# Performance work log

Hardware: AMD Instinct MI355X
Metric: run time of the kernel (lower is better)

The kernel has to match this reference:

```python
import jax, jax.numpy as jnp
import numpy as np

N = 100_000      # nodes
E = 1_250_000    # edges (avg degree ~12.5)
D_IN, D_H, D_OUT = 64, 64, 64


def setup_inputs() -> dict:
    key = jax.random.key(0)
    ks = jax.random.split(key, 7)
    x = jax.random.normal(ks[0], (N, D_IN), dtype=jnp.float32)
    edge_index = jax.random.randint(ks[1], (2, E), 0, N, dtype=jnp.int32)
    edge_weight = jax.random.uniform(ks[2], (E,), dtype=jnp.float32)
    # GCNConv linear weights: PyG lin stores [out, in], applied as x @ W.T; bias added after aggregation.
    W1 = jax.random.normal(ks[3], (D_H, D_IN), dtype=jnp.float32) * (1.0 / np.sqrt(D_IN))
    b1 = jax.random.normal(ks[4], (D_H,), dtype=jnp.float32) * 0.01
    W2 = jax.random.normal(ks[5], (D_OUT, D_H), dtype=jnp.float32) * (1.0 / np.sqrt(D_H))
    b2 = jax.random.normal(ks[6], (D_OUT,), dtype=jnp.float32) * 0.01
    return {"x": x, "edge_index": edge_index, "edge_weight": edge_weight,
            "W1": W1, "b1": b1, "W2": W2, "b2": b2}


def _gcn_conv(x, src, dst, w, W, b, n_nodes):
    # PyG GCNConv: add self-loops (weight 1), symmetric normalization, linear, scatter-add, +bias.
    deg = jax.ops.segment_sum(w, dst, num_segments=n_nodes) + 1.0  # +1 from self-loop
    dis = jnp.where(deg > 0, jax.lax.rsqrt(deg), 0.0)              # deg^{-1/2}
    coef = dis[src] * w * dis[dst]                                 # per-edge norm, [E]
    h = x @ W.T                                                    # [N, out]
    agg = jax.ops.segment_sum(h[src] * coef[:, None], dst, num_segments=n_nodes)
    agg = agg + h * (dis * dis)[:, None]                           # self-loop: dis_i * 1 * dis_i
    return agg + b


def reference(x, edge_index, edge_weight, W1, b1, W2, b2):
    n = x.shape[0]
    src, dst = edge_index[0], edge_index[1]
    h = _gcn_conv(x, src, dst, edge_weight, W1, b1, n)
    h = jax.nn.relu(h)
    # dropout p=0.0 -> identity
    return _gcn_conv(h, src, dst, edge_weight, W2, b2, n)
```

## Files before the change

### kernel.cpp

```cpp
#include <hip/hip_runtime.h>


typedef unsigned int u32;
typedef unsigned short u16;

#define NBKT 256
#define LSH 9
#define BNODES 512
#define SRCBITS 17
#define SRCMASK ((1u << SRCBITS) - 1u)

__device__ inline u16 f2bf(float f) {
  u32 u = __float_as_uint(f);
  u32 r = u + 0x7FFFu + ((u >> 16) & 1u);
  return (u16)(r >> 16);
}
__device__ inline float bf_lo(u32 p) { return __uint_as_float(p << 16); }
__device__ inline float bf_hi(u32 p) { return __uint_as_float(p & 0xFFFF0000u); }

__device__ inline u32 blockscan256_excl(u32 val, u32* wsum) {
  int lane = threadIdx.x & 63, wv = threadIdx.x >> 6;
  u32 inc = val;
  #pragma unroll
  for (int d = 1; d < 64; d <<= 1) {
    u32 t = __shfl_up(inc, d);
    if (lane >= d) inc += t;
  }
  if (lane == 63) wsum[wv] = inc;
  __syncthreads();
  u32 off = 0;
  #pragma unroll
  for (int i = 0; i < 4; ++i) if (i < wv) off += wsum[i];
  return off + inc - val;
}

__global__ void k_bin(const int* __restrict__ ei, u32* __restrict__ blockcnt,
                      int E, int chunk) {
  __shared__ u32 hist[NBKT];
  if (threadIdx.x < NBKT) hist[threadIdx.x] = 0u;
  __syncthreads();
  int e0 = blockIdx.x * chunk;
  int e1 = min(E, e0 + chunk);
  for (int e = e0 + (threadIdx.x << 1); e < e1; e += 512) {
    if (e + 1 < e1) {
      int2 dd = *(const int2*)(ei + E + e);
      atomicAdd(&hist[dd.x >> LSH], 1u);
      atomicAdd(&hist[dd.y >> LSH], 1u);
    } else {
      atomicAdd(&hist[ei[E + e] >> LSH], 1u);
    }
  }
  __syncthreads();
  if (threadIdx.x < NBKT)
    blockcnt[threadIdx.x * 256 + blockIdx.x] = hist[threadIdx.x];
}

__global__ void k_scan_rows(u32* __restrict__ blockcnt, u32* __restrict__ bucket_total) {
  int wid = blockIdx.x * 4 + (threadIdx.x >> 6);
  int lane = threadIdx.x & 63;
  u32* row = blockcnt + (size_t)wid * 256;
  uint4 v = ((uint4*)row)[lane];
  u32 s = v.x + v.y + v.z + v.w;
  u32 inc = s;
  #pragma unroll
  for (int d = 1; d < 64; d <<= 1) {
    u32 t = __shfl_up(inc, d);
    if (lane >= d) inc += t;
  }
  u32 excl = inc - s;
  uint4 o;
  o.x = excl; o.y = excl + v.x; o.z = o.y + v.y; o.w = o.z + v.z;
  ((uint4*)row)[lane] = o;
  if (lane == 63) bucket_total[wid] = inc;
}

__global__ void k_scan_buckets(const u32* __restrict__ bucket_total,
                               u32* __restrict__ bucket_start) {
  __shared__ u32 wsum[4];
  int t = threadIdx.x;
  u32 v = bucket_total[t];
  u32 excl = blockscan256_excl(v, wsum);
  bucket_start[t] = excl;
  if (t == 255) bucket_start[256] = excl + v;
}

__global__ __launch_bounds__(256, 4) void k_scatter_gemm(
    const int* __restrict__ ei, const float* __restrict__ w,
    const u32* __restrict__ blockcnt, const u32* __restrict__ bucket_start,
    uint2* __restrict__ bucketed,
    const float* __restrict__ X, const float* __restrict__ W,
    u16* __restrict__ H, int N, int E, int chunk) {
  __shared__ float Wt[64 * 65];
  __shared__ float Xs[16 * 64];
  __shared__ u32 base[NBKT];
  int tid = threadIdx.x;
  if ((int)blockIdx.x < 256) {
    if (tid < NBKT)
      base[tid] = blockcnt[(size_t)tid * 256 + blockIdx.x] + bucket_start[tid];
    __syncthreads();
    int e0 = blockIdx.x * chunk, e1 = min(E, e0 + chunk);
    for (int e = e0 + (tid << 1); e < e1; e += 512) {
      if (e + 1 < e1) {
        int2 ss = *(const int2*)(ei + e);
        int2 dd = *(const int2*)(ei + E + e);
        float2 wv = *(const float2*)(w + e);
        u32 p0 = atomicAdd(&base[dd.x >> LSH], 1u);
        u32 p1 = atomicAdd(&base[dd.y >> LSH], 1u);
        bucketed[p0] = make_uint2((u32)ss.x | ((u32)(dd.x & (BNODES - 1)) << SRCBITS),
                                  __float_as_uint(wv.x));
        bucketed[p1] = make_uint2((u32)ss.y | ((u32)(dd.y & (BNODES - 1)) << SRCBITS),
                                  __float_as_uint(wv.y));
      } else {
        int s = ei[e], d = ei[E + e];
        u32 pos = atomicAdd(&base[d >> LSH], 1u);
        bucketed[pos] = make_uint2((u32)s | ((u32)(d & (BNODES - 1)) << SRCBITS),
                                   __float_as_uint(w[e]));
      }
    }
    return;
  }
  int row0 = ((int)blockIdx.x - 256) * 16;
  if (row0 >= N) return;
  for (int i = tid; i < 4096; i += 256) Wt[(i & 63) * 65 + (i >> 6)] = W[i];
  {
    const float4* xsrc = (const float4*)(X + (size_t)row0 * 64);
    if (row0 + 16 <= N) {
      ((float4*)Xs)[tid] = xsrc[tid];
    } else {
      int r = tid >> 4;
      ((float4*)Xs)[tid] = (row0 + r < N) ? xsrc[tid]
                                          : make_float4(0.f, 0.f, 0.f, 0.f);
    }
  }
  __syncthreads();
  int lane = tid & 63, wv4 = tid >> 6;
  int rbase = wv4 * 4;
  float a0 = 0.f, a1 = 0.f, a2 = 0.f, a3 = 0.f;
  #pragma unroll 4
  for (int k4 = 0; k4 < 16; ++k4) {
    int k = k4 << 2;
    float w0 = Wt[k * 65 + lane], w1 = Wt[(k + 1) * 65 + lane];
    float w2 = Wt[(k + 2) * 65 + lane], w3 = Wt[(k + 3) * 65 + lane];
    float4 xa = *(const float4*)&Xs[(rbase + 0) * 64 + k];
    float4 xb = *(const float4*)&Xs[(rbase + 1) * 64 + k];
    float4 xc = *(const float4*)&Xs[(rbase + 2) * 64 + k];
    float4 xd = *(const float4*)&Xs[(rbase + 3) * 64 + k];
    a0 = fmaf(xa.x, w0, fmaf(xa.y, w1, fmaf(xa.z, w2, fmaf(xa.w, w3, a0))));
    a1 = fmaf(xb.x, w0, fmaf(xb.y, w1, fmaf(xb.z, w2, fmaf(xb.w, w3, a1))));
    a2 = fmaf(xc.x, w0, fmaf(xc.y, w1, fmaf(xc.z, w2, fmaf(xc.w, w3, a2))));
    a3 = fmaf(xd.x, w0, fmaf(xd.y, w1, fmaf(xd.z, w2, fmaf(xd.w, w3, a3))));
  }
  int row = row0 + rbase;
  if (row + 3 < N) {
    H[(size_t)row * 64 + lane]       = f2bf(a0);
    H[(size_t)(row + 1) * 64 + lane] = f2bf(a1);
    H[(size_t)(row + 2) * 64 + lane] = f2bf(a2);
    H[(size_t)(row + 3) * 64 + lane] = f2bf(a3);
  } else {
    if (row < N)     H[(size_t)row * 64 + lane]       = f2bf(a0);
    if (row + 1 < N) H[(size_t)(row + 1) * 64 + lane] = f2bf(a1);
    if (row + 2 < N) H[(size_t)(row + 2) * 64 + lane] = f2bf(a2);
    if (row + 3 < N) H[(size_t)(row + 3) * 64 + lane] = f2bf(a3);
  }
}

__global__ void k_statsfill(const uint2* __restrict__ bucketed,
                            const u32* __restrict__ bucket_start,
                            float* __restrict__ dis, int4* __restrict__ info,
                            int2* __restrict__ csr, u16* __restrict__ H, int N) {
  __shared__ u32 hist[BNODES];
  __shared__ u32 cur[BNODES];
  __shared__ float disl[BNODES];
  __shared__ u32 wsum[4];
  int b = blockIdx.x, tid = threadIdx.x;
  for (int i = tid; i < BNODES; i += 256) hist[i] = 0u;
  __syncthreads();
  u32 s0 = bucket_start[b], s1 = bucket_start[b + 1];
  for (u32 p = s0 + tid; p < s1; p += 256) {
    uint2 ed = bucketed[p];
    u32 local = ed.x >> SRCBITS;
    u32 wfix = (u32)(__uint_as_float(ed.y) * 262144.0f);
    atomicAdd(&hist[local], (1u << 24) | wfix);
  }
  __syncthreads();
  u32 h0 = hist[2 * tid], h1 = hist[2 * tid + 1];
  u32 c0 = h0 >> 24, c1 = h1 >> 24;
  u32 excl = blockscan256_excl(c0 + c1, wsum);
  float d0 = rsqrtf(1.0f + (float)(h0 & 0xFFFFFFu) * (1.0f / 262144.0f));
  float d1 = rsqrtf(1.0f + (float)(h1 & 0xFFFFFFu) * (1.0f / 262144.0f));
  cur[2 * tid] = excl;
  cur[2 * tid + 1] = excl + c0;
  disl[2 * tid] = d0;
  disl[2 * tid + 1] = d1;
  int n0 = b * BNODES + 2 * tid;
  if (n0 < N) {
    dis[n0] = d0;
    info[n0] = make_int4((int)(s0 + excl), (int)c0, __float_as_int(d0), 0);
  }
  if (n0 + 1 < N) {
    dis[n0 + 1] = d1;
    info[n0 + 1] = make_int4((int)(s0 + excl + c0), (int)c1, __float_as_int(d1), 0);
  }
  __syncthreads();
  for (u32 p = s0 + tid; p < s1; p += 256) {
    uint2 ed = bucketed[p];
    u32 local = ed.x >> SRCBITS;
    u32 pos = atomicAdd(&cur[local], 1u);
    csr[s0 + pos] = make_int2((int)(ed.x & SRCMASK), (int)ed.y);
  }
  uint2* Hv = (uint2*)H;
  for (int i = tid; i < BNODES * 16; i += 256) {
    int row = i >> 4;
    int node = b * BNODES + row;
    if (node >= N) break;
    float dv = disl[row];
    size_t idx = (size_t)node * 16 + (i & 15);
    uint2 v = Hv[idx];
    u32 lo = (u32)f2bf(bf_lo(v.x) * dv) | ((u32)f2bf(bf_hi(v.x) * dv) << 16);
    u32 hi = (u32)f2bf(bf_lo(v.y) * dv) | ((u32)f2bf(bf_hi(v.y) * dv) << 16);
    Hv[idx] = make_uint2(lo, hi);
  }
}

__global__ __launch_bounds__(256, 4) void k_gemm(
    const float* __restrict__ X, const float* __restrict__ W,
    const float* __restrict__ dis, u16* __restrict__ H, int N) {
  __shared__ float Wt[64 * 65];
  __shared__ float Xs[16 * 64];
  int tid = threadIdx.x;
  int row0 = blockIdx.x * 16;
  if (row0 >= N) return;
  for (int i = tid; i < 4096; i += 256) Wt[(i & 63) * 65 + (i >> 6)] = W[i];
  {
    const float4* xsrc = (const float4*)(X + (size_t)row0 * 64);
    if (row0 + 16 <= N) {
      ((float4*)Xs)[tid] = xsrc[tid];
    } else {
      int r = tid >> 4;
      ((float4*)Xs)[tid] = (row0 + r < N) ? xsrc[tid]
                                          : make_float4(0.f, 0.f, 0.f, 0.f);
    }
  }
  __syncthreads();
  int lane = tid & 63, wv = tid >> 6;
  int rbase = wv * 4;
  float a0 = 0.f, a1 = 0.f, a2 = 0.f, a3 = 0.f;
  #pragma unroll 4
  for (int k4 = 0; k4 < 16; ++k4) {
    int k = k4 << 2;
    float w0 = Wt[k * 65 + lane], w1 = Wt[(k + 1) * 65 + lane];
    float w2 = Wt[(k + 2) * 65 + lane], w3 = Wt[(k + 3) * 65 + lane];
    float4 xa = *(const float4*)&Xs[(rbase + 0) * 64 + k];
    float4 xb = *(const float4*)&Xs[(rbase + 1) * 64 + k];
    float4 xc = *(const float4*)&Xs[(rbase + 2) * 64 + k];
    float4 xd = *(const float4*)&Xs[(rbase + 3) * 64 + k];
    a0 = fmaf(xa.x, w0, fmaf(xa.y, w1, fmaf(xa.z, w2, fmaf(xa.w, w3, a0))));
    a1 = fmaf(xb.x, w0, fmaf(xb.y, w1, fmaf(xb.z, w2, fmaf(xb.w, w3, a1))));
    a2 = fmaf(xc.x, w0, fmaf(xc.y, w1, fmaf(xc.z, w2, fmaf(xc.w, w3, a2))));
    a3 = fmaf(xd.x, w0, fmaf(xd.y, w1, fmaf(xd.z, w2, fmaf(xd.w, w3, a3))));
  }
  int row = row0 + rbase;
  if (row + 3 < N) {
    float dv0 = dis[row], dv1 = dis[row + 1], dv2 = dis[row + 2], dv3 = dis[row + 3];
    H[(size_t)row * 64 + lane]       = f2bf(a0 * dv0);
    H[(size_t)(row + 1) * 64 + lane] = f2bf(a1 * dv1);
    H[(size_t)(row + 2) * 64 + lane] = f2bf(a2 * dv2);
    H[(size_t)(row + 3) * 64 + lane] = f2bf(a3 * dv3);
  } else {
    if (row < N)     H[(size_t)row * 64 + lane]       = f2bf(a0 * dis[row]);
    if (row + 1 < N) H[(size_t)(row + 1) * 64 + lane] = f2bf(a1 * dis[row + 1]);
    if (row + 2 < N) H[(size_t)(row + 2) * 64 + lane] = f2bf(a2 * dis[row + 2]);
    if (row + 3 < N) H[(size_t)(row + 3) * 64 + lane] = f2bf(a3 * dis[row + 3]);
  }
}

template <int RELU>
__global__ __launch_bounds__(256, 8) void k_aggregate(
    const u16* __restrict__ H, const int4* __restrict__ info,
    const int2* __restrict__ csr, const float* __restrict__ bias,
    float* __restrict__ Y, int N) {
  int tid = threadIdx.x;
  int node = blockIdx.x * 16 + (tid >> 4);
  int fid = (tid & 15) << 2;
  bool valid = node < N;
  int4 nfo = valid ? info[node] : make_int4(0, 0, 0, 0);
  int s0 = nfo.x, n = nfo.y;
  float d = __int_as_float(nfo.z);
  uint2 hs = valid ? *(const uint2*)(H + (size_t)node * 64 + fid)
                   : make_uint2(0u, 0u);
  float4 b4 = *(const float4*)(bias + fid);
  float4 acc = make_float4(0.f, 0.f, 0.f, 0.f);
  int nm1 = n - 1;
  for (int base = 0; base < n; base += 4) {
    int q1 = min(base + 1, nm1);
    int q2 = min(base + 2, nm1), q3 = min(base + 3, nm1);
    int2 c0 = csr[s0 + base];
    int2 c1 = csr[s0 + q1];
    int2 c2 = csr[s0 + q2];
    int2 c3 = csr[s0 + q3];
    uint2 h0 = *(const uint2*)(H + (size_t)c0.x * 64 + fid);
    uint2 h1 = *(const uint2*)(H + (size_t)c1.x * 64 + fid);
    uint2 h2 = *(const uint2*)(H + (size_t)c2.x * 64 + fid);
    uint2 h3 = *(const uint2*)(H + (size_t)c3.x * 64 + fid);
    float f0 = __int_as_float(c0.y);
    float f1 = (base + 1 < n) ? __int_as_float(c1.y) : 0.f;
    float f2 = (base + 2 < n) ? __int_as_float(c2.y) : 0.f;
    float f3 = (base + 3 < n) ? __int_as_float(c3.y) : 0.f;
    acc.x = fmaf(bf_lo(h0.x), f0, acc.x); acc.y = fmaf(bf_hi(h0.x), f0, acc.y);
    acc.z = fmaf(bf_lo(h0.y), f0, acc.z); acc.w = fmaf(bf_hi(h0.y), f0, acc.w);
    acc.x = fmaf(bf_lo(h1.x), f1, acc.x); acc.y = fmaf(bf_hi(h1.x), f1, acc.y);
    acc.z = fmaf(bf_lo(h1.y), f1, acc.z); acc.w = fmaf(bf_hi(h1.y), f1, acc.w);
    acc.x = fmaf(bf_lo(h2.x), f2, acc.x); acc.y = fmaf(bf_hi(h2.x), f2, acc.y);
    acc.z = fmaf(bf_lo(h2.y), f2, acc.z); acc.w = fmaf(bf_hi(h2.y), f2, acc.w);
    acc.x = fmaf(bf_lo(h3.x), f3, acc.x); acc.y = fmaf(bf_hi(h3.x), f3, acc.y);
    acc.z = fmaf(bf_lo(h3.y), f3, acc.z); acc.w = fmaf(bf_hi(h3.y), f3, acc.w);
  }
  if (valid) {
    acc.x = (acc.x + bf_lo(hs.x)) * d + b4.x;
    acc.y = (acc.y + bf_hi(hs.x)) * d + b4.y;
    acc.z = (acc.z + bf_lo(hs.y)) * d + b4.z;
    acc.w = (acc.w + bf_hi(hs.y)) * d + b4.w;
    if (RELU) {
      acc.x = fmaxf(acc.x, 0.f); acc.y = fmaxf(acc.y, 0.f);
      acc.z = fmaxf(acc.z, 0.f); acc.w = fmaxf(acc.w, 0.f);
    }
    *(float4*)(Y + (size_t)node * 64 + fid) = acc;
  }
}

extern "C" void kernel_launch(void* const* d_in, const int* in_sizes, int n_in,
                              void* d_out, int out_size, void* d_ws, size_t ws_size,
                              hipStream_t stream) {
  const float* x  = (const float*)d_in[0];
  const int*   ei = (const int*)d_in[1];
  const float* w  = (const float*)d_in[2];
  const float* W1 = (const float*)d_in[3];
  const float* b1 = (const float*)d_in[4];
  const float* W2 = (const float*)d_in[5];
  const float* b2 = (const float*)d_in[6];
  const int N = in_sizes[0] / 64;
  const int E = in_sizes[2];

  char* ws = (char*)d_ws;
  size_t off = 0;
  auto alloc = [&](size_t bytes) -> char* {
    char* p = ws + off;
    off = (off + bytes + 255) & ~(size_t)255;
    return p;
  };
  u32*   blockcnt     = (u32*)  alloc((size_t)NBKT * 256 * 4);
  u32*   bucket_total = (u32*)  alloc((size_t)NBKT * 4);
  u32*   bucket_start = (u32*)  alloc((size_t)(NBKT + 1) * 4);
  uint2* bucketed     = (uint2*)alloc((size_t)E * 8);
  int2*  csr          = (int2*) alloc((size_t)E * 8);
  float* dis          = (float*)alloc((size_t)N * 4);
  int4*  info         = (int4*) alloc((size_t)N * 16);
  u16*   h1           = (u16*)  alloc((size_t)N * 64 * 2);
  u16*   h2           = (u16*)  alloc((size_t)N * 64 * 2);
  float* ybuf         = (float*)d_out;

  const int chunk = ((E + 511) / 512) * 2;
  const int nbG = (N + 15) / 16;
  const int nbA = (N + 15) / 16;
  const int nbB = (N + BNODES - 1) >> LSH;

  k_bin<<<256, 256, 0, stream>>>(ei, blockcnt, E, chunk);
  k_scan_rows<<<NBKT / 4, 256, 0, stream>>>(blockcnt, bucket_total);
  k_scan_buckets<<<1, 256, 0, stream>>>(bucket_total, bucket_start);
  k_scatter_gemm<<<256 + nbG, 256, 0, stream>>>(ei, w, blockcnt, bucket_start,
                                                bucketed, x, W1, h1, N, E, chunk);
  k_statsfill<<<nbB, 256, 0, stream>>>(bucketed, bucket_start, dis, info, csr, h1, N);

  k_aggregate<1><<<nbA, 256, 0, stream>>>(h1, info, csr, b1, ybuf, N);
  k_gemm<<<nbG, 256, 0, stream>>>(ybuf, W2, dis, h2, N);
  k_aggregate<0><<<nbA, 256, 0, stream>>>(h2, info, csr, b2, (float*)d_out, N);
}
```

Measured before the change: 245.2 us.

## Compute degree by global atomics, drop scans, fuse aggregate with second GEMM

Degrees are now accumulated with global float atomics in the binning pass, and bucket offsets come from atomic counters into fixed-capacity (CAP) bucket slots, so both scan kernels go away. Degree scaling moves into the first GEMM epilogue, which removes the separate H rescale pass in statsfill. The first aggregation is fused with the second GEMM through shared memory, so the fp32 intermediate no longer makes a round trip through global memory. In exchange it adds contention on global atomics and risks overflow if any bucket holds more than CAP edges; it also introduces nondeterministic edge ordering and an occupancy change.

After: 286.5 us. 16.8% more time.

```diff
diff --git a/kernel.cpp b/kernel.cpp
--- a/kernel.cpp
+++ b/kernel.cpp
@@ -7,6 +7,7 @@
 #define NBKT 256
 #define LSH 9
 #define BNODES 512
+#define CAP 8192
 #define SRCBITS 17
 #define SRCMASK ((1u << SRCBITS) - 1u)
 
@@ -34,8 +35,9 @@
   return off + inc - val;
 }
 
-__global__ void k_bin(const int* __restrict__ ei, u32* __restrict__ blockcnt,
-                      int E, int chunk) {
+__global__ void k_deg_bin(const int* __restrict__ ei, const float* __restrict__ w,
+                          float* __restrict__ deg, u32* __restrict__ bucket_cnt,
+                          u32* __restrict__ blockbase, int E, int chunk) {
   __shared__ u32 hist[NBKT];
   if (threadIdx.x < NBKT) hist[threadIdx.x] = 0u;
   __syncthreads();
@@ -44,59 +46,36 @@
   for (int e = e0 + (threadIdx.x << 1); e < e1; e += 512) {
     if (e + 1 < e1) {
       int2 dd = *(const int2*)(ei + E + e);
+      float2 wv = *(const float2*)(w + e);
       atomicAdd(&hist[dd.x >> LSH], 1u);
       atomicAdd(&hist[dd.y >> LSH], 1u);
+      atomicAdd(&deg[dd.x], wv.x);
+      atomicAdd(&deg[dd.y], wv.y);
     } else {
-      atomicAdd(&hist[ei[E + e] >> LSH], 1u);
+      int d = ei[E + e];
+      atomicAdd(&hist[d >> LSH], 1u);
+      atomicAdd(&deg[d], w[e]);
     }
   }
   __syncthreads();
   if (threadIdx.x < NBKT)
-    blockcnt[threadIdx.x * 256 + blockIdx.x] = hist[threadIdx.x];
-}
-
-__global__ void k_scan_rows(u32* __restrict__ blockcnt, u32* __restrict__ bucket_total) {
-  int wid = blockIdx.x * 4 + (threadIdx.x >> 6);
-  int lane = threadIdx.x & 63;
-  u32* row = blockcnt + (size_t)wid * 256;
-  uint4 v = ((uint4*)row)[lane];
-  u32 s = v.x + v.y + v.z + v.w;
-  u32 inc = s;
-  #pragma unroll
-  for (int d = 1; d < 64; d <<= 1) {
-    u32 t = __shfl_up(inc, d);
-    if (lane >= d) inc += t;
-  }
-  u32 excl = inc - s;
-  uint4 o;
-  o.x = excl; o.y = excl + v.x; o.z = o.y + v.y; o.w = o.z + v.z;
-  ((uint4*)row)[lane] = o;
-  if (lane == 63) bucket_total[wid] = inc;
-}
-
-__global__ void k_scan_buckets(const u32* __restrict__ bucket_total,
-                               u32* __restrict__ bucket_start) {
-  __shared__ u32 wsum[4];
-  int t = threadIdx.x;
-  u32 v = bucket_total[t];
-  u32 excl = blockscan256_excl(v, wsum);
-  bucket_start[t] = excl;
-  if (t == 255) bucket_start[256] = excl + v;
+    blockbase[threadIdx.x * 256 + blockIdx.x] =
+        atomicAdd(&bucket_cnt[threadIdx.x], hist[threadIdx.x]);
 }
 
 __global__ __launch_bounds__(256, 4) void k_scatter_gemm(
     const int* __restrict__ ei, const float* __restrict__ w,
-    const u32* __restrict__ blockcnt, const u32* __restrict__ bucket_start,
+    const u32* __restrict__ blockbase,
     uint2* __restrict__ bucketed,
     const float* __restrict__ X, const float* __restrict__ W,
-    u16* __restrict__ H, int N, int E, int chunk) {
+    const float* __restrict__ deg, u16* __restrict__ H, int N, int E, int chunk) {
   __shared__ float Wt[64 * 65];
   __shared__ float Xs[16 * 64];
   __shared__ u32 base[NBKT];
   int tid = threadIdx.x;
   if ((int)blockIdx.x < 256) {
     if (tid < NBKT)
-      base[tid] = blockcnt[(size_t)tid * 256 + blockIdx.x] + bucket_start[tid];
+      base[tid] = (u32)tid * CAP + blockbase[tid * 256 + blockIdx.x];
     __syncthreads();
     int e0 = blockIdx.x * chunk, e1 = min(E, e0 + chunk);
     for (int e = e0 + (tid << 1); e < e1; e += 512) {
@@ -152,108 +131,124 @@
   }
   int row = row0 + rbase;
   if (row + 3 < N) {
-    H[(size_t)row * 64 + lane]       = f2bf(a0);
-    H[(size_t)(row + 1) * 64 + lane] = f2bf(a1);
-    H[(size_t)(row + 2) * 64 + lane] = f2bf(a2);
-    H[(size_t)(row + 3) * 64 + lane] = f2bf(a3);
+    float dv0 = rsqrtf(1.f + deg[row]);
+    float dv1 = rsqrtf(1.f + deg[row + 1]);
+    float dv2 = rsqrtf(1.f + deg[row + 2]);
+    float dv3 = rsqrtf(1.f + deg[row + 3]);
+    H[(size_t)row * 64 + lane]       = f2bf(a0 * dv0);
+    H[(size_t)(row + 1) * 64 + lane] = f2bf(a1 * dv1);
+    H[(size_t)(row + 2) * 64 + lane] = f2bf(a2 * dv2);
+    H[(size_t)(row + 3) * 64 + lane] = f2bf(a3 * dv3);
   } else {
-    if (row < N)     H[(size_t)row * 64 + lane]       = f2bf(a0);
-    if (row + 1 < N) H[(size_t)(row + 1) * 64 + lane] = f2bf(a1);
-    if (row + 2 < N) H[(size_t)(row + 2) * 64 + lane] = f2bf(a2);
-    if (row + 3 < N) H[(size_t)(row + 3) * 64 + lane] = f2bf(a3);
+    if (row < N)     H[(size_t)row * 64 + lane]       = f2bf(a0 * rsqrtf(1.f + deg[row]));
+    if (row + 1 < N) H[(size_t)(row + 1) * 64 + lane] = f2bf(a1 * rsqrtf(1.f + deg[row + 1]));
+    if (row + 2 < N) H[(size_t)(row + 2) * 64 + lane] = f2bf(a2 * rsqrtf(1.f + deg[row + 2]));
+    if (row + 3 < N) H[(size_t)(row + 3) * 64 + lane] = f2bf(a3 * rsqrtf(1.f + deg[row + 3]));
   }
 }
 
 __global__ void k_statsfill(const uint2* __restrict__ bucketed,
-                            const u32* __restrict__ bucket_start,
-                            float* __restrict__ dis, int4* __restrict__ info,
-                            int2* __restrict__ csr, u16* __restrict__ H, int N) {
+                            const u32* __restrict__ bucket_cnt,
+                            const float* __restrict__ deg,
+                            int4* __restrict__ info, int2* __restrict__ csr, int N) {
   __shared__ u32 hist[BNODES];
   __shared__ u32 cur[BNODES];
-  __shared__ float disl[BNODES];
   __shared__ u32 wsum[4];
   int b = blockIdx.x, tid = threadIdx.x;
   for (int i = tid; i < BNODES; i += 256) hist[i] = 0u;
   __syncthreads();
-  u32 s0 = bucket_start[b], s1 = bucket_start[b + 1];
+  u32 s0 = (u32)b * CAP, s1 = s0 + bucket_cnt[b];
+  for (u32 p = s0 + tid; p < s1; p += 256)
+    atomicAdd(&hist[bucketed[p].x >> SRCBITS], 1u);
+  __syncthreads();
+  u32 c0 = hist[2 * tid], c1 = hist[2 * tid + 1];
+  u32 excl = blockscan256_excl(c0 + c1, wsum);
+  cur[2 * tid] = excl;
+  cur[2 * tid + 1] = excl + c0;
+  int n0 = b * BNODES + 2 * tid;
+  if (n0 < N) {
+    float d0 = rsqrtf(1.f + deg[n0]);
+    info[n0] = make_int4((int)(s0 + excl), (int)c0, __float_as_int(d0), 0);
+  }
+  if (n0 + 1 < N) {
+    float d1 = rsqrtf(1.f + deg[n0 + 1]);
+    info[n0 + 1] = make_int4((int)(s0 + excl + c0), (int)c1, __float_as_int(d1), 0);
+  }
+  __syncthreads();
   for (u32 p = s0 + tid; p < s1; p += 256) {
     uint2 ed = bucketed[p];
-    u32 local = ed.x >> SRCBITS;
-    u32 wfix = (u32)(__uint_as_float(ed.y) * 262144.0f);
-    atomicAdd(&hist[local], (1u << 24) | wfix);
-  }
-  __syncthreads();
-  u32 h0 = hist[2 * tid], h1 = hist[2 * tid + 1];
-  u32 c0 = h0 >> 24, c1 = h1 >> 24;
-  u32 excl = blockscan256_excl(c0 + c1, wsum);
-  float d0 = rsqrtf(1.0f + (float)(h0 & 0xFFFFFFu) * (1.0f / 262144.0f));
-  float d1 = rsqrtf(1.0f + (float)(h1 & 0xFFFFFFu) * (1.0f / 262144.0f));
-  cur[2 * tid] = excl;
-  cur[2 * tid + 1] = excl + c0;
-  disl[2 * tid] = d0;
-  disl[2 * tid + 1] = d1;
-  int n0 = b * BNODES + 2 * tid;
-  if (n0 < N) {
-    dis[n0] = d0;
-    info[n0] = make_int4((int)(s0 + excl), (int)c0, __float_as_int(d0), 0);
-  }
-  if (n0 + 1 < N) {
-    dis[n0 + 1] = d1;
-    info[n0 + 1] = make_int4((int)(s0 + excl + c0), (int)c1, __float_as_int(d1), 0);
-  }
-  __syncthreads();
-  for (u32 p = s0 + tid; p < s1; p += 256) {
-    uint2 ed = bucketed[p];
-    u32 local = ed.x >> SRCBITS;
-    u32 pos = atomicAdd(&cur[local], 1u);
+    u32 pos = atomicAdd(&cur[ed.x >> SRCBITS], 1u);
     csr[s0 + pos] = make_int2((int)(ed.x & SRCMASK), (int)ed.y);
   }
-  uint2* Hv = (uint2*)H;
-  for (int i = tid; i < BNODES * 16; i += 256) {
-    int row = i >> 4;
-    int node = b * BNODES + row;
-    if (node >= N) break;
-    float dv = disl[row];
-    size_t idx = (size_t)node * 16 + (i & 15);
-    uint2 v = Hv[idx];
-    u32 lo = (u32)f2bf(bf_lo(v.x) * dv) | ((u32)f2bf(bf_hi(v.x) * dv) << 16);
-    u32 hi = (u32)f2bf(bf_lo(v.y) * dv) | ((u32)f2bf(bf_hi(v.y) * dv) << 16);
-    Hv[idx] = make_uint2(lo, hi);
-  }
-}
-
-__global__ __launch_bounds__(256, 4) void k_gemm(
-    const float* __restrict__ X, const float* __restrict__ W,
-    const float* __restrict__ dis, u16* __restrict__ H, int N) {
+}
+
+__global__ __launch_bounds__(256, 6) void k_agg_gemm(
+    const u16* __restrict__ H, const int4* __restrict__ info,
+    const int2* __restrict__ csr, const float* __restrict__ bias,
+    const float* __restrict__ W2, const float* __restrict__ deg,
+    u16* __restrict__ H2, int N) {
   __shared__ float Wt[64 * 65];
-  __shared__ float Xs[16 * 64];
+  __shared__ float Ys[16 * 64];
   int tid = threadIdx.x;
-  int row0 = blockIdx.x * 16;
-  if (row0 >= N) return;
-  for (int i = tid; i < 4096; i += 256) Wt[(i & 63) * 65 + (i >> 6)] = W[i];
-  {
-    const float4* xsrc = (const float4*)(X + (size_t)row0 * 64);
-    if (row0 + 16 <= N) {
-      ((float4*)Xs)[tid] = xsrc[tid];
-    } else {
-      int r = tid >> 4;
-      ((float4*)Xs)[tid] = (row0 + r < N) ? xsrc[tid]
-                                          : make_float4(0.f, 0.f, 0.f, 0.f);
-    }
-  }
+  for (int i = tid; i < 4096; i += 256) Wt[(i & 63) * 65 + (i >> 6)] = W2[i];
+  int node = blockIdx.x * 16 + (tid >> 4);
+  int fid = (tid & 15) << 2;
+  bool valid = node < N;
+  int4 nfo = valid ? info[node] : make_int4(0, 0, 0, 0);
+  int s0 = nfo.x, n = nfo.y;
+  float d = __int_as_float(nfo.z);
+  uint2 hs = valid ? *(const uint2*)(H + (size_t)node * 64 + fid)
+                   : make_uint2(0u, 0u);
+  float4 b4 = *(const float4*)(bias + fid);
+  float4 acc = make_float4(0.f, 0.f, 0.f, 0.f);
+  int nm1 = n - 1;
+  for (int base = 0; base < n; base += 4) {
+    int q1 = min(base + 1, nm1);
+    int q2 = min(base + 2, nm1), q3 = min(base + 3, nm1);
+    int2 c0 = csr[s0 + base];
+    int2 c1 = csr[s0 + q1];
+    int2 c2 = csr[s0 + q2];
+    int2 c3 = csr[s0 + q3];
+    uint2 h0 = *(const uint2*)(H + (size_t)c0.x * 64 + fid);
+    uint2 h1 = *(const uint2*)(H + (size_t)c1.x * 64 + fid);
+    uint2 h2 = *(const uint2*)(H + (size_t)c2.x * 64 + fid);
+    uint2 h3 = *(const uint2*)(H + (size_t)c3.x * 64 + fid);
+    float f0 = __int_as_float(c0.y);
+    float f1 = (base + 1 < n) ? __int_as_float(c1.y) : 0.f;
+    float f2 = (base + 2 < n) ? __int_as_float(c2.y) : 0.f;
+    float f3 = (base + 3 < n) ? __int_as_float(c3.y) : 0.f;
+    acc.x = fmaf(bf_lo(h0.x), f0, acc.x); acc.y = fmaf(bf_hi(h0.x), f0, acc.y);
+    acc.z = fmaf(bf_lo(h0.y), f0, acc.z); acc.w = fmaf(bf_hi(h0.y), f0, acc.w);
+    acc.x = fmaf(bf_lo(h1.x), f1, acc.x); acc.y = fmaf(bf_hi(h1.x), f1, acc.y);
+    acc.z = fmaf(bf_lo(h1.y), f1, acc.z); acc.w = fmaf(bf_hi(h1.y), f1, acc.w);
+    acc.x = fmaf(bf_lo(h2.x), f2, acc.x); acc.y = fmaf(bf_hi(h2.x), f2, acc.y);
+    acc.z = fmaf(bf_lo(h2.y), f2, acc.z); acc.w = fmaf(bf_hi(h2.y), f2, acc.w);
+    acc.x = fmaf(bf_lo(h3.x), f3, acc.x); acc.y = fmaf(bf_hi(h3.x), f3, acc.y);
+    acc.z = fmaf(bf_lo(h3.y), f3, acc.z); acc.w = fmaf(bf_hi(h3.y), f3, acc.w);
+  }
+  if (valid) {
+    acc.x = fmaxf((acc.x + bf_lo(hs.x)) * d + b4.x, 0.f);
+    acc.y = fmaxf((acc.y + bf_hi(hs.x)) * d + b4.y, 0.f);
+    acc.z = fmaxf((acc.z + bf_lo(hs.y)) * d + b4.z, 0.f);
+    acc.w = fmaxf((acc.w + bf_hi(hs.y)) * d + b4.w, 0.f);
+  } else {
+    acc = make_float4(0.f, 0.f, 0.f, 0.f);
+  }
+  *(float4*)&Ys[(tid >> 4) * 64 + fid] = acc;
   __syncthreads();
   int lane = tid & 63, wv = tid >> 6;
   int rbase = wv * 4;
+  int row0 = blockIdx.x * 16;
   float a0 = 0.f, a1 = 0.f, a2 = 0.f, a3 = 0.f;
   #pragma unroll 4
   for (int k4 = 0; k4 < 16; ++k4) {
     int k = k4 << 2;
     float w0 = Wt[k * 65 + lane], w1 = Wt[(k + 1) * 65 + lane];
     float w2 = Wt[(k + 2) * 65 + lane], w3 = Wt[(k + 3) * 65 + lane];
-    float4 xa = *(const float4*)&Xs[(rbase + 0) * 64 + k];
-    float4 xb = *(const float4*)&Xs[(rbase + 1) * 64 + k];
-    float4 xc = *(const float4*)&Xs[(rbase + 2) * 64 + k];
-    float4 xd = *(const float4*)&Xs[(rbase + 3) * 64 + k];
+    float4 xa = *(const float4*)&Ys[(rbase + 0) * 64 + k];
+    float4 xb = *(const float4*)&Ys[(rbase + 1) * 64 + k];
+    float4 xc = *(const float4*)&Ys[(rbase + 2) * 64 + k];
+    float4 xd = *(const float4*)&Ys[(rbase + 3) * 64 + k];
     a0 = fmaf(xa.x, w0, fmaf(xa.y, w1, fmaf(xa.z, w2, fmaf(xa.w, w3, a0))));
     a1 = fmaf(xb.x, w0, fmaf(xb.y, w1, fmaf(xb.z, w2, fmaf(xb.w, w3, a1))));
     a2 = fmaf(xc.x, w0, fmaf(xc.y, w1, fmaf(xc.z, w2, fmaf(xc.w, w3, a2))));
@@ -261,21 +256,23 @@
   }
   int row = row0 + rbase;
   if (row + 3 < N) {
-    float dv0 = dis[row], dv1 = dis[row + 1], dv2 = dis[row + 2], dv3 = dis[row + 3];
-    H[(size_t)row * 64 + lane]       = f2bf(a0 * dv0);
-    H[(size_t)(row + 1) * 64 + lane] = f2bf(a1 * dv1);
-    H[(size_t)(row + 2) * 64 + lane] = f2bf(a2 * dv2);
-    H[(size_t)(row + 3) * 64 + lane] = f2bf(a3 * dv3);
+    float dv0 = rsqrtf(1.f + deg[row]);
+    float dv1 = rsqrtf(1.f + deg[row + 1]);
+    float dv2 = rsqrtf(1.f + deg[row + 2]);
+    float dv3 = rsqrtf(1.f + deg[row + 3]);
+    H2[(size_t)row * 64 + lane]       = f2bf(a0 * dv0);
+    H2[(size_t)(row + 1) * 64 + lane] = f2bf(a1 * dv1);
+    H2[(size_t)(row + 2) * 64 + lane] = f2bf(a2 * dv2);
+    H2[(size_t)(row + 3) * 64 + lane] = f2bf(a3 * dv3);
   } else {
-    if (row < N)     H[(size_t)row * 64 + lane]       = f2bf(a0 * dis[row]);
-    if (row + 1 < N) H[(size_t)(row + 1) * 64 + lane] = f2bf(a1 * dis[row + 1]);
-    if (row + 2 < N) H[(size_t)(row + 2) * 64 + lane] = f2bf(a2 * dis[row + 2]);
-    if (row + 3 < N) H[(size_t)(row + 3) * 64 + lane] = f2bf(a3 * dis[row + 3]);
-  }
-}
-
-template <int RELU>
-__global__ __launch_bounds__(256, 8) void k_aggregate(
+    if (row < N)     H2[(size_t)row * 64 + lane]       = f2bf(a0 * rsqrtf(1.f + deg[row]));
+    if (row + 1 < N) H2[(size_t)(row + 1) * 64 + lane] = f2bf(a1 * rsqrtf(1.f + deg[row + 1]));
+    if (row + 2 < N) H2[(size_t)(row + 2) * 64 + lane] = f2bf(a2 * rsqrtf(1.f + deg[row + 2]));
+    if (row + 3 < N) H2[(size_t)(row + 3) * 64 + lane] = f2bf(a3 * rsqrtf(1.f + deg[row + 3]));
+  }
+}
+
+__global__ __launch_bounds__(256, 8) void k_aggregate2(
     const u16* __restrict__ H, const int4* __restrict__ info,
     const int2* __restrict__ csr, const float* __restrict__ bias,
     float* __restrict__ Y, int N) {
@@ -320,10 +317,6 @@
     acc.y = (acc.y + bf_hi(hs.x)) * d + b4.y;
     acc.z = (acc.z + bf_lo(hs.y)) * d + b4.z;
     acc.w = (acc.w + bf_hi(hs.y)) * d + b4.w;
-    if (RELU) {
-      acc.x = fmaxf(acc.x, 0.f); acc.y = fmaxf(acc.y, 0.f);
-      acc.z = fmaxf(acc.z, 0.f); acc.w = fmaxf(acc.w, 0.f);
-    }
     *(float4*)(Y + (size_t)node * 64 + fid) = acc;
   }
 }
@@ -348,30 +341,26 @@
     off = (off + bytes + 255) & ~(size_t)255;
     return p;
   };
-  u32*   blockcnt     = (u32*)  alloc((size_t)NBKT * 256 * 4);
-  u32*   bucket_total = (u32*)  alloc((size_t)NBKT * 4);
-  u32*   bucket_start = (u32*)  alloc((size_t)(NBKT + 1) * 4);
-  uint2* bucketed     = (uint2*)alloc((size_t)E * 8);
-  int2*  csr          = (int2*) alloc((size_t)E * 8);
-  float* dis          = (float*)alloc((size_t)N * 4);
+  float* deg          = (float*)alloc((size_t)N * 4);
+  u32*   bucket_cnt   = (u32*)  alloc((size_t)NBKT * 4);
+  size_t zero_bytes   = (size_t)((char*)(bucket_cnt + NBKT) - (char*)deg);
+  u32*   blockbase    = (u32*)  alloc((size_t)NBKT * 256 * 4);
+  uint2* bucketed     = (uint2*)alloc((size_t)NBKT * CAP * 8);
+  int2*  csr          = (int2*) alloc((size_t)NBKT * CAP * 8);
   int4*  info         = (int4*) alloc((size_t)N * 16);
   u16*   h1           = (u16*)  alloc((size_t)N * 64 * 2);
   u16*   h2           = (u16*)  alloc((size_t)N * 64 * 2);
-  float* ybuf         = (float*)d_out;
 
   const int chunk = ((E + 511) / 512) * 2;
   const int nbG = (N + 15) / 16;
   const int nbA = (N + 15) / 16;
   const int nbB = (N + BNODES - 1) >> LSH;
 
-  k_bin<<<256, 256, 0, stream>>>(ei, blockcnt, E, chunk);
-  k_scan_rows<<<NBKT / 4, 256, 0, stream>>>(blockcnt, bucket_total);
-  k_scan_buckets<<<1, 256, 0, stream>>>(bucket_total, bucket_start);
-  k_scatter_gemm<<<256 + nbG, 256, 0, stream>>>(ei, w, blockcnt, bucket_start,
-                                                bucketed, x, W1, h1, N, E, chunk);
-  k_statsfill<<<nbB, 256, 0, stream>>>(bucketed, bucket_start, dis, info, csr, h1, N);
-
-  k_aggregate<1><<<nbA, 256, 0, stream>>>(h1, info, csr, b1, ybuf, N);
-  k_gemm<<<nbG, 256, 0, stream>>>(ybuf, W2, dis, h2, N);
-  k_aggregate<0><<<nbA, 256, 0, stream>>>(h2, info, csr, b2, (float*)d_out, N);
-}
+  hipMemsetAsync(deg, 0, zero_bytes, stream);
+  k_deg_bin<<<256, 256, 0, stream>>>(ei, w, deg, bucket_cnt, blockbase, E, chunk);
+  k_scatter_gemm<<<256 + nbG, 256, 0, stream>>>(ei, w, blockbase, bucketed,
+                                                x, W1, deg, h1, N, E, chunk);
+  k_statsfill<<<nbB, 256, 0, stream>>>(bucketed, bucket_cnt, deg, info, csr, N);
+  k_agg_gemm<<<nbA, 256, 0, stream>>>(h1, info, csr, b1, W2, deg, h2, N);
+  k_aggregate2<<<nbA, 256, 0, stream>>>(h2, info, csr, b2, (float*)d_out, N);
+}
```
